# Kernel optimization log

Measured on AMD Instinct MI355X. Metric: run time of the kernel, lower is better.

Reference implementation:

```python
import jax, jax.numpy as jnp
import numpy as np

# config derived from init_kwargs: batch_sizes=[2048,2048], rs=[32,128], num_adapters=[32,32]
B1, B2, MULT = 2048, 2048, 4            # group1 tokens (r_mult=1), group2 tokens (r_mult=128/32=4)
IN_F, OUT_F, R_MIN = 4096, 4096, 32
NA1, NA2 = 32, 32
N_SPLIT_ADAPTERS = NA1 + NA2 * MULT      # 160 rank-min slices
LORA_BATCH = B1 + B2 * MULT              # 10240 gathered rows


def setup_inputs() -> dict:
    key = jax.random.key(0)
    k1, k2, k3, k4, k5 = jax.random.split(key, 5)
    x = jax.random.normal(k1, (B1 + B2, 1, IN_F), dtype=jnp.float16)
    lora_A = (jax.random.normal(k2, (N_SPLIT_ADAPTERS, IN_F, R_MIN), dtype=jnp.float16) * jnp.float16(0.02))
    lora_B = (jax.random.normal(k3, (N_SPLIT_ADAPTERS, R_MIN, OUT_F), dtype=jnp.float16) * jnp.float16(0.02))
    # group1: one row per token; group2: each token repeated MULT times (rank split)
    xids = jnp.concatenate([
        jnp.arange(B1, dtype=jnp.int32),
        jnp.repeat(jnp.arange(B1, B1 + B2, dtype=jnp.int32), MULT),
    ])
    # group1 adapters occupy slice ids [0, NA1); group2 adapter j occupies NA1 + j*MULT .. +MULT-1
    w1 = jax.random.randint(k4, (B1,), 0, NA1, dtype=jnp.int32)
    j = jax.random.randint(k5, (B2,), 0, NA2, dtype=jnp.int32)
    w2 = ((jnp.int32(NA1) + j * MULT)[:, None] + jnp.arange(MULT, dtype=jnp.int32)[None, :]).reshape(-1)
    wids = jnp.concatenate([w1, w2])
    return {"x": x, "xids": xids, "wids": wids, "lora_A": lora_A, "lora_B": lora_B}


def reference(x, xids, wids, lora_A, lora_B):
    xg = jnp.take(x, xids, axis=0)          # (L, 1, IN_F)
    A = jnp.take(lora_A, wids, axis=0)      # (L, IN_F, R_MIN)
    Bw = jnp.take(lora_B, wids, axis=0)     # (L, R_MIN, OUT_F)
    y = jnp.einsum('lpi,lir->lpr', xg, A)   # (L, 1, R_MIN)
    y = jnp.einsum('lpr,lro->lpo', y, Bw) * 2.0  # (L, 1, OUT_F), scaling factor 2.0
    # split + sum combine: group1 passes through, group2 sums each block of MULT rank-slices
    z1 = y[:B1]                                          # (B1, 1, OUT_F)
    z2 = y[B1:].reshape(B2, MULT, 1, OUT_F).sum(axis=1)  # (B2, 1, OUT_F)
    return jnp.concatenate([z1, z2], axis=0)             # (B1+B2, 1, OUT_F)
```

## Files before the change

### kernel.cpp

```cpp
#include <hip/hip_runtime.h>

#define IN_F   4096
#define OUT_F  4096
#define RK     32
#define NB1    2048
#define LBATCH 10240
#define MAXB   2048
#define TILES  4
#define LRK    (LBATCH * RK)

typedef __attribute__((ext_vector_type(2))) __fp16 h2;
typedef __attribute__((ext_vector_type(8))) __fp16 h8;
typedef __attribute__((ext_vector_type(4))) float  f4;


__global__ __launch_bounds__(1024) void bin_rows(const int* __restrict__ wids,
                                                 int* __restrict__ cnt,
                                                 int* __restrict__ list) {
    __shared__ int lc[64];
    int t = threadIdx.x;
    if (t < 64) lc[t] = 0;
    __syncthreads();
    for (int it = t; it < 4096; it += 1024) {
        int b, v;
        if (it < NB1) { b = wids[it]; v = it; }
        else { int i = it - NB1; b = 32 + ((wids[NB1 + 4 * i] - 32) >> 2); v = i; }
        int p = atomicAdd(&lc[b], 1);
        list[b * MAXB + p] = v;
    }
    __syncthreads();
    if (t < 64) cnt[t] = lc[t];
}

template<bool P2>
__device__ __forceinline__ void s1_body(const float* __restrict__ x,
                                        const float* __restrict__ A,
                                        float* __restrict__ slab,
                                        __fp16 (*At)[128][40],
                                        const int* rowid,
                                        int g, int k0, int nsteps, int tz, int n) {
    constexpr int NT  = P2 ? 8 : 2;
    constexpr int NTK = P2 ? 2 : 1;

    int t = threadIdx.x, lane = t & 63, w = t >> 6, m = lane & 15, kg = lane >> 4;

    int xr = rowid[16 * w + m];
    const float* xb = x + (size_t)(P2 ? NB1 + xr : xr) * IN_F + k0 + kg * 8;

    int tkp[NTK], tc0[NTK];
    const float* ap[NTK];
    #pragma unroll
    for (int p = 0; p < NTK; ++p) {
        int tau = P2 ? (t + 256 * p) : (t & 127);
        int kp  = P2 ? (tau >> 5) : (tau >> 3);
        int c4  = P2 ? (tau & 31) : (tau & 7);
        int c0  = 4 * c4;
        tkp[p] = kp; tc0[p] = c0;
        int ad  = P2 ? (32 + 4 * g + (c0 >> 5)) : g;
        ap[p] = A + ((size_t)ad * IN_F + k0 + 2 * kp) * RK + (c0 & 31);
    }

    f4 acc[NT];
    #pragma unroll
    for (int ct = 0; ct < NT; ++ct) acc[ct] = (f4){0.f, 0.f, 0.f, 0.f};

    f4 xf0 = *(const f4*)xb, xf1 = *(const f4*)(xb + 4);
    f4 a0[NTK], a1[NTK];
    #pragma unroll
    for (int p = 0; p < NTK; ++p) { a0[p] = *(const f4*)ap[p]; a1[p] = *(const f4*)(ap[p] + RK); }
    #pragma unroll
    for (int p = 0; p < NTK; ++p) {
        int k = 2 * tkp[p];
        #pragma unroll
        for (int j = 0; j < 4; ++j) {
            int c  = tc0[p] + j;
            int kb = (k >> 3) ^ ((c >> 3) & 3);
            *(h2*)&At[0][c][kb * 8 + (k & 7)] = __builtin_amdgcn_cvt_pkrtz(a0[p][j], a1[p][j]);
        }
    }
    __syncthreads();

    for (int s = 0; s < nsteps; ++s) {
        int  b    = s & 1;
        bool more = (s + 1 < nsteps);
        f4 nx0, nx1, n0[NTK], n1[NTK];
        if (more) {
            nx0 = *(const f4*)(xb + (size_t)(s + 1) * 32);
            nx1 = *(const f4*)(xb + (size_t)(s + 1) * 32 + 4);
            #pragma unroll
            for (int p = 0; p < NTK; ++p) {
                const float* q = ap[p] + (size_t)(s + 1) * 32 * RK;
                n0[p] = *(const f4*)q; n1[p] = *(const f4*)(q + RK);
            }
        }
        h8 xa;
        {
            union { h8 v8; h2 h[4]; } u;
            u.h[0] = __builtin_amdgcn_cvt_pkrtz(xf0.x, xf0.y);
            u.h[1] = __builtin_amdgcn_cvt_pkrtz(xf0.z, xf0.w);
            u.h[2] = __builtin_amdgcn_cvt_pkrtz(xf1.x, xf1.y);
            u.h[3] = __builtin_amdgcn_cvt_pkrtz(xf1.z, xf1.w);
            xa = u.v8;
        }
        #pragma unroll
        for (int ct = 0; ct < NT; ++ct) {
            int c  = ct * 16 + m;
            int kb = kg ^ ((c >> 3) & 3);
            h8 bf  = *(const h8*)&At[b][c][kb * 8];
            acc[ct] = __builtin_amdgcn_mfma_f32_16x16x32_f16(xa, bf, acc[ct], 0, 0, 0);
        }
        if (more) {
            #pragma unroll
            for (int p = 0; p < NTK; ++p) {
                int k = 2 * tkp[p];
                #pragma unroll
                for (int j = 0; j < 4; ++j) {
                    int c  = tc0[p] + j;
                    int kb = (k >> 3) ^ ((c >> 3) & 3);
                    *(h2*)&At[b ^ 1][c][kb * 8 + (k & 7)] = __builtin_amdgcn_cvt_pkrtz(n0[p][j], n1[p][j]);
                }
            }
            xf0 = nx0; xf1 = nx1;
        }
        __syncthreads();
    }

    #pragma unroll
    for (int q = 0; q < 4; ++q) {
        int br = 16 * w + 4 * kg + q;
        int it = 64 * tz + br;
        if (it < n) {
            int rid = rowid[br];
            #pragma unroll
            for (int ct = 0; ct < NT; ++ct) {
                int c = ct * 16 + m;
                size_t off = P2 ? ((size_t)(NB1 + 4 * rid + (c >> 5)) * RK + (c & 31))
                                : ((size_t)rid * RK + c);
                slab[off] = acc[ct][q];
            }
        }
    }
}

__global__ __launch_bounds__(256, 4) void s1_all(const float* __restrict__ x,
                                                 const float* __restrict__ A,
                                                 const int*   __restrict__ cnt,
                                                 const int*   __restrict__ list,
                                                 float*       __restrict__ slabs,
                                                 int nsteps) {
    __shared__ __align__(16) __fp16 At[2][128][40];
    __shared__ int rowid[64];
    int g  = blockIdx.x;
    int tz = blockIdx.z;
    int n  = cnt[g];
    if (64 * tz >= n) return;
    if (threadIdx.x < 64) {
        int it = 64 * tz + threadIdx.x;
        rowid[threadIdx.x] = list[g * MAXB + (it < n ? it : n - 1)];
    }
    __syncthreads();
    int k0 = blockIdx.y * nsteps * 32;
    float* slab = slabs + (size_t)blockIdx.y * LRK;
    if (g < 32) s1_body<false>(x, A, slab, At, rowid, g, k0, nsteps, tz, n);
    else        s1_body<true >(x, A, slab, At, rowid, g - 32, k0, nsteps, tz, n);
}

template<bool P2>
__device__ __forceinline__ void s2_body(const float* __restrict__ slabs, int nslab,
                                        const float* __restrict__ B,
                                        float* __restrict__ out,
                                        __fp16 (*Bt)[40],
                                        const int* rowid,
                                        int g, int ot0, int tz, int n) {
    constexpr int NS  = P2 ? 4 : 1;
    constexpr int NPH = P2 ? 16 : 4;

    int t = threadIdx.x, lane = t & 63, w = t >> 6, m = lane & 15, kg = lane >> 4;
    int rid0 = rowid[16 * w + m];

    h8 rf[NS];
    #pragma unroll
    for (int kc = 0; kc < NS; ++kc) {
        size_t ro = P2 ? (size_t)(NB1 + 4 * rid0 + kc) : (size_t)rid0;
        const float* rp = slabs + ro * RK + kg * 8;
        f4 sa = *(const f4*)rp, sb = *(const f4*)(rp + 4);
        for (int s = 1; s < nslab; ++s) {
            const float* q2 = rp + (size_t)s * LRK;
            sa += *(const f4*)q2; sb += *(const f4*)(q2 + 4);
        }
        h8 f;
        f[0] = (__fp16)sa.x; f[1] = (__fp16)sa.y; f[2] = (__fp16)sa.z; f[3] = (__fp16)sa.w;
        f[4] = (__fp16)sb.x; f[5] = (__fp16)sb.y; f[6] = (__fp16)sb.z; f[7] = (__fp16)sb.w;
        rf[kc] = f;
    }

    int oc = t & 127, kh = t >> 7;

    float v[16], vn[16];
    {
        int a = P2 ? (32 + 4 * g) : g;
        const float* s0 = B + ((size_t)a * RK + kh * 16) * OUT_F + (size_t)ot0 * 128 + oc;
        #pragma unroll
        for (int q = 0; q < 16; ++q) v[q] = s0[q * OUT_F];
    }

    f4 acc[8];
    #pragma unroll
    for (int ct = 0; ct < 8; ++ct) acc[ct] = (f4){0.f, 0.f, 0.f, 0.f};

    #pragma unroll
    for (int ph = 0; ph < NPH; ++ph) {
        int oti = P2 ? (ph >> 2) : ph;
        int kc  = P2 ? (ph & 3) : 0;
        __syncthreads();
        #pragma unroll
        for (int q = 0; q < 8; ++q)
            *(h2*)&Bt[oc][kh * 16 + 2 * q] = __builtin_amdgcn_cvt_pkrtz(v[2 * q], v[2 * q + 1]);
        if (ph + 1 < NPH) {
            int noti = P2 ? ((ph + 1) >> 2) : (ph + 1);
            int nkc  = P2 ? ((ph + 1) & 3) : 0;
            int a = P2 ? (32 + 4 * g + nkc) : g;
            const float* sn = B + ((size_t)a * RK + kh * 16) * OUT_F + (size_t)(ot0 + noti) * 128 + oc;
            #pragma unroll
            for (int q = 0; q < 16; ++q) vn[q] = sn[q * OUT_F];
        }
        __syncthreads();
        #pragma unroll
        for (int ct = 0; ct < 8; ++ct) {
            h8 bf = *(const h8*)&Bt[ct * 16 + m][kg * 8];
            acc[ct] = __builtin_amdgcn_mfma_f32_16x16x32_f16(rf[kc], bf, acc[ct], 0, 0, 0);
        }
        if (kc == NS - 1) {
            #pragma unroll
            for (int q = 0; q < 4; ++q) {
                int br = 16 * w + 4 * kg + q;
                int it = 64 * tz + br;
                if (it < n) {
                    int orow = P2 ? (NB1 + rowid[br]) : rowid[br];
                    float* op = out + (size_t)orow * OUT_F + (size_t)(ot0 + oti) * 128 + m;
                    #pragma unroll
                    for (int ct = 0; ct < 8; ++ct)
                        op[ct * 16] = 2.f * acc[ct][q];
                }
            }
            #pragma unroll
            for (int ct = 0; ct < 8; ++ct) acc[ct] = (f4){0.f, 0.f, 0.f, 0.f};
        }
        #pragma unroll
        for (int q = 0; q < 16; ++q) v[q] = vn[q];
    }
}

__global__ __launch_bounds__(256, 3) void s2_all(const float* __restrict__ slabs,
                                                 int nslab,
                                                 const float* __restrict__ B,
                                                 const int*   __restrict__ cnt,
                                                 const int*   __restrict__ list,
                                                 float*       __restrict__ out) {
    __shared__ __align__(16) __fp16 Bt[128][40];
    __shared__ int rowid[64];
    int g   = blockIdx.x;
    int ot0 = blockIdx.y * 4;
    int tz  = blockIdx.z;
    int n   = cnt[g];
    if (64 * tz >= n) return;
    if (threadIdx.x < 64) {
        int it = 64 * tz + threadIdx.x;
        rowid[threadIdx.x] = list[g * MAXB + (it < n ? it : n - 1)];
    }
    __syncthreads();
    if (g < 32) s2_body<false>(slabs, nslab, B, out, Bt, rowid, g, ot0, tz, n);
    else        s2_body<true >(slabs, nslab, B, out, Bt, rowid, g - 32, ot0, tz, n);
}

extern "C" void kernel_launch(void* const* d_in, const int* in_sizes, int n_in,
                              void* d_out, int out_size, void* d_ws, size_t ws_size,
                              hipStream_t stream) {
    const float* x    = (const float*)d_in[0];
    const int*   wids = (const int*)  d_in[2];
    const float* A    = (const float*)d_in[3];
    const float* Bm   = (const float*)d_in[4];
    float* out = (float*)d_out;

    int* wsI  = (int*)d_ws;
    int* cnt  = wsI;
    int* list = wsI + 64;
    float* slabs = (float*)(list + 64 * MAXB);

    size_t fixed = (size_t)(64 + 64 * MAXB) * sizeof(int);
    int ks = 8;
    while (ks > 1 && fixed + (size_t)ks * LRK * sizeof(float) > ws_size) ks >>= 1;
    int nsteps = 128 / ks;

    bin_rows<<<dim3(1), dim3(1024), 0, stream>>>(wids, cnt, list);
    s1_all<<<dim3(64, ks, TILES), dim3(256), 0, stream>>>(x, A, cnt, list, slabs, nsteps);
    s2_all<<<dim3(64, 8, TILES), dim3(256), 0, stream>>>(slabs, ks, Bm, cnt, list, out);
}
```

Before: 292.8 us.

## Restructure LoRA kernels: per-wave row tiles, separate reduction, register-resident B weights

Replaces the fixed 64-row-tile grid for both stages. The first stage now gives each wave its own row tiles and its own LDS buffer, with one block per rank slice and k-chunk, and loads x for a 512-wide k span into registers. A new reduceR kernel sums the k-split partials into a half-precision rank buffer. The second stage keeps its B-weight fragments in registers for the whole block and loops over all rows in the bucket, so B is loaded once per block instead of once per row tile. This adds a kernel launch and leaves the work per block uneven when bucket sizes differ.

```diff
diff --git a/kernel.cpp b/kernel.cpp
--- a/kernel.cpp
+++ b/kernel.cpp
@@ -4,9 +4,8 @@
 #define OUT_F  4096
 #define RK     32
 #define NB1    2048
+#define MAXB   2048
 #define LBATCH 10240
-#define MAXB   2048
-#define TILES  4
 #define LRK    (LBATCH * RK)
 
 typedef __attribute__((ext_vector_type(2))) __fp16 h2;
@@ -32,245 +31,186 @@
     if (t < 64) cnt[t] = lc[t];
 }
 
-template<bool P2>
-__device__ __forceinline__ void s1_body(const float* __restrict__ x,
-                                        const float* __restrict__ A,
-                                        float* __restrict__ slab,
-                                        __fp16 (*At)[128][40],
-                                        const int* rowid,
-                                        int g, int k0, int nsteps, int tz, int n) {
-    constexpr int NT  = P2 ? 8 : 2;
-    constexpr int NTK = P2 ? 2 : 1;
-
-    int t = threadIdx.x, lane = t & 63, w = t >> 6, m = lane & 15, kg = lane >> 4;
-
-    int xr = rowid[16 * w + m];
-    const float* xb = x + (size_t)(P2 ? NB1 + xr : xr) * IN_F + k0 + kg * 8;
-
-    int tkp[NTK], tc0[NTK];
-    const float* ap[NTK];
-    #pragma unroll
-    for (int p = 0; p < NTK; ++p) {
-        int tau = P2 ? (t + 256 * p) : (t & 127);
-        int kp  = P2 ? (tau >> 5) : (tau >> 3);
-        int c4  = P2 ? (tau & 31) : (tau & 7);
-        int c0  = 4 * c4;
-        tkp[p] = kp; tc0[p] = c0;
-        int ad  = P2 ? (32 + 4 * g + (c0 >> 5)) : g;
-        ap[p] = A + ((size_t)ad * IN_F + k0 + 2 * kp) * RK + (c0 & 31);
-    }
-
-    f4 acc[NT];
-    #pragma unroll
-    for (int ct = 0; ct < NT; ++ct) acc[ct] = (f4){0.f, 0.f, 0.f, 0.f};
-
-    f4 xf0 = *(const f4*)xb, xf1 = *(const f4*)(xb + 4);
-    f4 a0[NTK], a1[NTK];
-    #pragma unroll
-    for (int p = 0; p < NTK; ++p) { a0[p] = *(const f4*)ap[p]; a1[p] = *(const f4*)(ap[p] + RK); }
-    #pragma unroll
-    for (int p = 0; p < NTK; ++p) {
-        int k = 2 * tkp[p];
+__device__ __forceinline__ void lda(const float* __restrict__ As, int s,
+                                    int kp0, int c40, f4 L[2][2]) {
+    #pragma unroll
+    for (int p = 0; p < 2; ++p) {
+        const float* q = As + ((size_t)s * 32 + 2 * (kp0 + 8 * p)) * RK + c40;
+        L[p][0] = *(const f4*)q;
+        L[p][1] = *(const f4*)(q + RK);
+    }
+}
+__device__ __forceinline__ void wra(__fp16 (*dst)[40], int kp0, int c40,
+                                    const f4 L[2][2]) {
+    #pragma unroll
+    for (int p = 0; p < 2; ++p) {
+        int k = 2 * (kp0 + 8 * p);
         #pragma unroll
         for (int j = 0; j < 4; ++j) {
-            int c  = tc0[p] + j;
+            int c  = c40 + j;
             int kb = (k >> 3) ^ ((c >> 3) & 3);
-            *(h2*)&At[0][c][kb * 8 + (k & 7)] = __builtin_amdgcn_cvt_pkrtz(a0[p][j], a1[p][j]);
-        }
-    }
-    __syncthreads();
-
-    for (int s = 0; s < nsteps; ++s) {
-        int  b    = s & 1;
-        bool more = (s + 1 < nsteps);
-        f4 nx0, nx1, n0[NTK], n1[NTK];
-        if (more) {
-            nx0 = *(const f4*)(xb + (size_t)(s + 1) * 32);
-            nx1 = *(const f4*)(xb + (size_t)(s + 1) * 32 + 4);
+            *(h2*)&dst[c][kb * 8 + (k & 7)] =
+                __builtin_amdgcn_cvt_pkrtz(L[p][0][j], L[p][1][j]);
+        }
+    }
+}
+
+template<int KS>
+__global__ __launch_bounds__(256, 3) void s1(const float* __restrict__ x,
+                                             const float* __restrict__ A,
+                                             const int* __restrict__ cnt,
+                                             const int* __restrict__ list,
+                                             float* __restrict__ slabs) {
+    constexpr int KCH = IN_F / KS;
+    constexpr int NSC = KCH / 512;
+    __shared__ __fp16 At[4][2][32][40];
+    int lane = threadIdx.x & 63, wv = threadIdx.x >> 6;
+    int bx = blockIdx.x;
+    int p2 = bx >= 32;
+    int u  = p2 ? ((bx - 32) & 31) : bx;
+    int mm = p2 ? ((bx - 32) >> 5) : 0;
+    int vb  = p2 ? (32 + 4 * u + mm) : bx;
+    int bkt = p2 ? (32 + u) : bx;
+    int n = cnt[bkt];
+    if (wv * 16 >= n) return;
+    const int* lst = list + bkt * MAXB;
+    int m = lane & 15, kg = lane >> 4;
+    int kc = blockIdx.y;
+    int k0 = kc * KCH;
+    const float* Ab = A + ((size_t)vb * IN_F + k0) * RK;
+    float* slab = slabs + (size_t)kc * LRK;
+    int kp0 = lane >> 3;
+    int c40 = (lane & 7) * 4;
+    __fp16 (*buf)[32][40] = At[wv];
+
+    for (int rt = wv; rt * 16 < n; rt += 4) {
+        int it  = rt * 16 + m;
+        int rid = lst[it < n ? it : n - 1];
+        const float* xb = x + (size_t)(rid + (p2 ? NB1 : 0)) * IN_F + k0 + kg * 8;
+
+        f4 acc0 = {0.f, 0.f, 0.f, 0.f}, acc1 = {0.f, 0.f, 0.f, 0.f};
+        for (int sc = 0; sc < NSC; ++sc) {
+            const float* xs = xb + sc * 512;
+            const float* As = Ab + (size_t)sc * 512 * RK;
+            h8 xf[16];
             #pragma unroll
-            for (int p = 0; p < NTK; ++p) {
-                const float* q = ap[p] + (size_t)(s + 1) * 32 * RK;
-                n0[p] = *(const f4*)q; n1[p] = *(const f4*)(q + RK);
-            }
-        }
-        h8 xa;
-        {
-            union { h8 v8; h2 h[4]; } u;
-            u.h[0] = __builtin_amdgcn_cvt_pkrtz(xf0.x, xf0.y);
-            u.h[1] = __builtin_amdgcn_cvt_pkrtz(xf0.z, xf0.w);
-            u.h[2] = __builtin_amdgcn_cvt_pkrtz(xf1.x, xf1.y);
-            u.h[3] = __builtin_amdgcn_cvt_pkrtz(xf1.z, xf1.w);
-            xa = u.v8;
-        }
-        #pragma unroll
-        for (int ct = 0; ct < NT; ++ct) {
-            int c  = ct * 16 + m;
-            int kb = kg ^ ((c >> 3) & 3);
-            h8 bf  = *(const h8*)&At[b][c][kb * 8];
-            acc[ct] = __builtin_amdgcn_mfma_f32_16x16x32_f16(xa, bf, acc[ct], 0, 0, 0);
-        }
-        if (more) {
+            for (int s = 0; s < 16; ++s) {
+                f4 x0 = *(const f4*)(xs + s * 32);
+                f4 x1 = *(const f4*)(xs + s * 32 + 4);
+                union { h8 v; h2 h[4]; } u2;
+                u2.h[0] = __builtin_amdgcn_cvt_pkrtz(x0.x, x0.y);
+                u2.h[1] = __builtin_amdgcn_cvt_pkrtz(x0.z, x0.w);
+                u2.h[2] = __builtin_amdgcn_cvt_pkrtz(x1.x, x1.y);
+                u2.h[3] = __builtin_amdgcn_cvt_pkrtz(x1.z, x1.w);
+                xf[s] = u2.v;
+            }
+            f4 L0[2][2], L1[2][2];
+            lda(As, 0, kp0, c40, L0);
+            wra(buf[0], kp0, c40, L0);
+            lda(As, 1, kp0, c40, L1);
             #pragma unroll
-            for (int p = 0; p < NTK; ++p) {
-                int k = 2 * tkp[p];
+            for (int s = 0; s < 16; ++s) {
+                h8 bf0, bf1;
+                { int c = m;      int kb = kg ^ ((c >> 3) & 3); bf0 = *(const h8*)&buf[s & 1][c][kb * 8]; }
+                { int c = 16 + m; int kb = kg ^ ((c >> 3) & 3); bf1 = *(const h8*)&buf[s & 1][c][kb * 8]; }
+                if (s + 2 < 16) lda(As, s + 2, kp0, c40, (s & 1) ? L1 : L0);
+                acc0 = __builtin_amdgcn_mfma_f32_16x16x32_f16(xf[s], bf0, acc0, 0, 0, 0);
+                acc1 = __builtin_amdgcn_mfma_f32_16x16x32_f16(xf[s], bf1, acc1, 0, 0, 0);
+                if (s + 1 < 16) wra(buf[(s + 1) & 1], kp0, c40, (s & 1) ? L0 : L1);
+            }
+        }
+        #pragma unroll
+        for (int q = 0; q < 4; ++q) {
+            int itq = rt * 16 + 4 * kg + q;
+            if (itq < n) {
+                int ridq = lst[itq];
+                int srow = p2 ? (NB1 + 4 * ridq + mm) : ridq;
+                float* sp = slab + (size_t)srow * RK + m;
+                sp[0]  = acc0[q];
+                sp[16] = acc1[q];
+            }
+        }
+    }
+}
+
+template<int KS>
+__global__ __launch_bounds__(256) void reduceR(const float* __restrict__ slabs,
+                                               __fp16* __restrict__ Rh) {
+    int i = (blockIdx.x * 256 + threadIdx.x) * 8;
+    f4 a = *(const f4*)(slabs + i);
+    f4 b = *(const f4*)(slabs + i + 4);
+    #pragma unroll
+    for (int s = 1; s < KS; ++s) {
+        a += *(const f4*)(slabs + (size_t)s * LRK + i);
+        b += *(const f4*)(slabs + (size_t)s * LRK + i + 4);
+    }
+    h8 o;
+    o[0] = (__fp16)a.x; o[1] = (__fp16)a.y; o[2] = (__fp16)a.z; o[3] = (__fp16)a.w;
+    o[4] = (__fp16)b.x; o[5] = (__fp16)b.y; o[6] = (__fp16)b.z; o[7] = (__fp16)b.w;
+    *(h8*)(Rh + i) = o;
+}
+
+__global__ __launch_bounds__(256, 4) void s2(const __fp16* __restrict__ Rh,
+                                             const float* __restrict__ B,
+                                             const int* __restrict__ cnt,
+                                             const int* __restrict__ list,
+                                             float* __restrict__ out) {
+    int lane = threadIdx.x & 63, wv = threadIdx.x >> 6;
+    int g   = blockIdx.x;
+    int oct = blockIdx.y * 4 + wv;
+    int p2  = g >= 32;
+    int n = cnt[g];
+    if (n == 0) return;
+    const int* lst = list + g * MAXB;
+    int m = lane & 15, kg = lane >> 4;
+    int oc0 = oct * 32;
+    int nkc = p2 ? 4 : 1;
+
+    h8 bf[4][2];
+    #pragma unroll
+    for (int kcb = 0; kcb < 4; ++kcb) {
+        if (kcb < nkc) {
+            int a = p2 ? (32 + 4 * (g - 32) + kcb) : g;
+            const float* Bb = B + ((size_t)a * RK + kg * 8) * OUT_F + oc0 + m;
+            #pragma unroll
+            for (int ct = 0; ct < 2; ++ct) {
+                union { h8 v; h2 h[4]; } u2;
                 #pragma unroll
-                for (int j = 0; j < 4; ++j) {
-                    int c  = tc0[p] + j;
-                    int kb = (k >> 3) ^ ((c >> 3) & 3);
-                    *(h2*)&At[b ^ 1][c][kb * 8 + (k & 7)] = __builtin_amdgcn_cvt_pkrtz(n0[p][j], n1[p][j]);
+                for (int jj = 0; jj < 4; ++jj) {
+                    float e0 = Bb[(size_t)(2 * jj) * OUT_F + ct * 16];
+                    float e1 = Bb[(size_t)(2 * jj + 1) * OUT_F + ct * 16];
+                    u2.h[jj] = __builtin_amdgcn_cvt_pkrtz(e0, e1);
                 }
-            }
-            xf0 = nx0; xf1 = nx1;
-        }
-        __syncthreads();
-    }
-
-    #pragma unroll
-    for (int q = 0; q < 4; ++q) {
-        int br = 16 * w + 4 * kg + q;
-        int it = 64 * tz + br;
-        if (it < n) {
-            int rid = rowid[br];
-            #pragma unroll
-            for (int ct = 0; ct < NT; ++ct) {
-                int c = ct * 16 + m;
-                size_t off = P2 ? ((size_t)(NB1 + 4 * rid + (c >> 5)) * RK + (c & 31))
-                                : ((size_t)rid * RK + c);
-                slab[off] = acc[ct][q];
-            }
-        }
-    }
-}
-
-__global__ __launch_bounds__(256, 4) void s1_all(const float* __restrict__ x,
-                                                 const float* __restrict__ A,
-                                                 const int*   __restrict__ cnt,
-                                                 const int*   __restrict__ list,
-                                                 float*       __restrict__ slabs,
-                                                 int nsteps) {
-    __shared__ __align__(16) __fp16 At[2][128][40];
-    __shared__ int rowid[64];
-    int g  = blockIdx.x;
-    int tz = blockIdx.z;
-    int n  = cnt[g];
-    if (64 * tz >= n) return;
-    if (threadIdx.x < 64) {
-        int it = 64 * tz + threadIdx.x;
-        rowid[threadIdx.x] = list[g * MAXB + (it < n ? it : n - 1)];
-    }
-    __syncthreads();
-    int k0 = blockIdx.y * nsteps * 32;
-    float* slab = slabs + (size_t)blockIdx.y * LRK;
-    if (g < 32) s1_body<false>(x, A, slab, At, rowid, g, k0, nsteps, tz, n);
-    else        s1_body<true >(x, A, slab, At, rowid, g - 32, k0, nsteps, tz, n);
-}
-
-template<bool P2>
-__device__ __forceinline__ void s2_body(const float* __restrict__ slabs, int nslab,
-                                        const float* __restrict__ B,
-                                        float* __restrict__ out,
-                                        __fp16 (*Bt)[40],
-                                        const int* rowid,
-                                        int g, int ot0, int tz, int n) {
-    constexpr int NS  = P2 ? 4 : 1;
-    constexpr int NPH = P2 ? 16 : 4;
-
-    int t = threadIdx.x, lane = t & 63, w = t >> 6, m = lane & 15, kg = lane >> 4;
-    int rid0 = rowid[16 * w + m];
-
-    h8 rf[NS];
-    #pragma unroll
-    for (int kc = 0; kc < NS; ++kc) {
-        size_t ro = P2 ? (size_t)(NB1 + 4 * rid0 + kc) : (size_t)rid0;
-        const float* rp = slabs + ro * RK + kg * 8;
-        f4 sa = *(const f4*)rp, sb = *(const f4*)(rp + 4);
-        for (int s = 1; s < nslab; ++s) {
-            const float* q2 = rp + (size_t)s * LRK;
-            sa += *(const f4*)q2; sb += *(const f4*)(q2 + 4);
-        }
-        h8 f;
-        f[0] = (__fp16)sa.x; f[1] = (__fp16)sa.y; f[2] = (__fp16)sa.z; f[3] = (__fp16)sa.w;
-        f[4] = (__fp16)sb.x; f[5] = (__fp16)sb.y; f[6] = (__fp16)sb.z; f[7] = (__fp16)sb.w;
-        rf[kc] = f;
-    }
-
-    int oc = t & 127, kh = t >> 7;
-
-    float v[16], vn[16];
-    {
-        int a = P2 ? (32 + 4 * g) : g;
-        const float* s0 = B + ((size_t)a * RK + kh * 16) * OUT_F + (size_t)ot0 * 128 + oc;
-        #pragma unroll
-        for (int q = 0; q < 16; ++q) v[q] = s0[q * OUT_F];
-    }
-
-    f4 acc[8];
-    #pragma unroll
-    for (int ct = 0; ct < 8; ++ct) acc[ct] = (f4){0.f, 0.f, 0.f, 0.f};
-
-    #pragma unroll
-    for (int ph = 0; ph < NPH; ++ph) {
-        int oti = P2 ? (ph >> 2) : ph;
-        int kc  = P2 ? (ph & 3) : 0;
-        __syncthreads();
-        #pragma unroll
-        for (int q = 0; q < 8; ++q)
-            *(h2*)&Bt[oc][kh * 16 + 2 * q] = __builtin_amdgcn_cvt_pkrtz(v[2 * q], v[2 * q + 1]);
-        if (ph + 1 < NPH) {
-            int noti = P2 ? ((ph + 1) >> 2) : (ph + 1);
-            int nkc  = P2 ? ((ph + 1) & 3) : 0;
-            int a = P2 ? (32 + 4 * g + nkc) : g;
-            const float* sn = B + ((size_t)a * RK + kh * 16) * OUT_F + (size_t)(ot0 + noti) * 128 + oc;
-            #pragma unroll
-            for (int q = 0; q < 16; ++q) vn[q] = sn[q * OUT_F];
-        }
-        __syncthreads();
-        #pragma unroll
-        for (int ct = 0; ct < 8; ++ct) {
-            h8 bf = *(const h8*)&Bt[ct * 16 + m][kg * 8];
-            acc[ct] = __builtin_amdgcn_mfma_f32_16x16x32_f16(rf[kc], bf, acc[ct], 0, 0, 0);
-        }
-        if (kc == NS - 1) {
-            #pragma unroll
-            for (int q = 0; q < 4; ++q) {
-                int br = 16 * w + 4 * kg + q;
-                int it = 64 * tz + br;
-                if (it < n) {
-                    int orow = P2 ? (NB1 + rowid[br]) : rowid[br];
-                    float* op = out + (size_t)orow * OUT_F + (size_t)(ot0 + oti) * 128 + m;
-                    #pragma unroll
-                    for (int ct = 0; ct < 8; ++ct)
-                        op[ct * 16] = 2.f * acc[ct][q];
-                }
-            }
-            #pragma unroll
-            for (int ct = 0; ct < 8; ++ct) acc[ct] = (f4){0.f, 0.f, 0.f, 0.f};
-        }
-        #pragma unroll
-        for (int q = 0; q < 16; ++q) v[q] = vn[q];
-    }
-}
-
-__global__ __launch_bounds__(256, 3) void s2_all(const float* __restrict__ slabs,
-                                                 int nslab,
-                                                 const float* __restrict__ B,
-                                                 const int*   __restrict__ cnt,
-                                                 const int*   __restrict__ list,
-                                                 float*       __restrict__ out) {
-    __shared__ __align__(16) __fp16 Bt[128][40];
-    __shared__ int rowid[64];
-    int g   = blockIdx.x;
-    int ot0 = blockIdx.y * 4;
-    int tz  = blockIdx.z;
-    int n   = cnt[g];
-    if (64 * tz >= n) return;
-    if (threadIdx.x < 64) {
-        int it = 64 * tz + threadIdx.x;
-        rowid[threadIdx.x] = list[g * MAXB + (it < n ? it : n - 1)];
-    }
-    __syncthreads();
-    if (g < 32) s2_body<false>(slabs, nslab, B, out, Bt, rowid, g, ot0, tz, n);
-    else        s2_body<true >(slabs, nslab, B, out, Bt, rowid, g - 32, ot0, tz, n);
+                bf[kcb][ct] = u2.v;
+            }
+        }
+    }
+
+    for (int rt = 0; rt * 16 < n; ++rt) {
+        int it = rt * 16 + m;
+        int ridm = lst[it < n ? it : n - 1];
+        f4 acc0 = {0.f, 0.f, 0.f, 0.f}, acc1 = {0.f, 0.f, 0.f, 0.f};
+        #pragma unroll
+        for (int kcb = 0; kcb < 4; ++kcb) {
+            if (kcb < nkc) {
+                int rrow = p2 ? (NB1 + 4 * ridm + kcb) : ridm;
+                h8 rf = *(const h8*)(Rh + (size_t)rrow * RK + kg * 8);
+                acc0 = __builtin_amdgcn_mfma_f32_16x16x32_f16(rf, bf[kcb][0], acc0, 0, 0, 0);
+                acc1 = __builtin_amdgcn_mfma_f32_16x16x32_f16(rf, bf[kcb][1], acc1, 0, 0, 0);
+            }
+        }
+        #pragma unroll
+        for (int q = 0; q < 4; ++q) {
+            int itq = rt * 16 + 4 * kg + q;
+            if (itq < n) {
+                int ridq = lst[itq];
+                int orow = p2 ? (NB1 + ridq) : ridq;
+                float* op = out + (size_t)orow * OUT_F + oc0 + m;
+                op[0]  = 2.f * acc0[q];
+                op[16] = 2.f * acc1[q];
+            }
+        }
+    }
 }
 
 extern "C" void kernel_launch(void* const* d_in, const int* in_sizes, int n_in,
@@ -285,14 +225,19 @@
     int* wsI  = (int*)d_ws;
     int* cnt  = wsI;
     int* list = wsI + 64;
-    float* slabs = (float*)(list + 64 * MAXB);
-
-    size_t fixed = (size_t)(64 + 64 * MAXB) * sizeof(int);
-    int ks = 8;
-    while (ks > 1 && fixed + (size_t)ks * LRK * sizeof(float) > ws_size) ks >>= 1;
-    int nsteps = 128 / ks;
+    __fp16* Rh  = (__fp16*)(list + 64 * MAXB);
+    float* slabs = (float*)((char*)Rh + (size_t)LRK * sizeof(__fp16));
+
+    size_t fixed = (size_t)(64 + 64 * MAXB) * sizeof(int) + (size_t)LRK * sizeof(__fp16);
+    int ks = (ws_size >= fixed + (size_t)8 * LRK * sizeof(float)) ? 8 : 4;
 
     bin_rows<<<dim3(1), dim3(1024), 0, stream>>>(wids, cnt, list);
-    s1_all<<<dim3(64, ks, TILES), dim3(256), 0, stream>>>(x, A, cnt, list, slabs, nsteps);
-    s2_all<<<dim3(64, 8, TILES), dim3(256), 0, stream>>>(slabs, ks, Bm, cnt, list, out);
-}
+    if (ks == 8) {
+        s1<8><<<dim3(160, 8), dim3(256), 0, stream>>>(x, A, cnt, list, slabs);
+        reduceR<8><<<dim3(LRK / 2048), dim3(256), 0, stream>>>(slabs, Rh);
+    } else {
+        s1<4><<<dim3(160, 4), dim3(256), 0, stream>>>(x, A, cnt, list, slabs);
+        reduceR<4><<<dim3(LRK / 2048), dim3(256), 0, stream>>>(slabs, Rh);
+    }
+    s2<<<dim3(64, 32), dim3(256), 0, stream>>>(Rh, Bm, cnt, list, out);
+}
```

Result: slower. 328.9 us (+12.3%).
